# Kernel tuning notes

Hardware: AMD Instinct MI355X
Metric: run time of the kernel (lower is better)

Reference implementation:

```python
import jax, jax.numpy as jnp
import numpy as np

EMBED_DIM = 1024
NUM_HEADS = 16
NUM_GROUPS = 4
HEAD_DIM = EMBED_DIM // NUM_HEADS
REPEAT = NUM_HEADS // NUM_GROUPS
MAX_TIME = 128
MAX_FREQ = 8


def build_relative_index(q_len, k_len, freq_size=MAX_FREQ, max_time=MAX_TIME, max_freq=MAX_FREQ):
    # static (numpy) construction; shapes are compile-time constants under jit
    q_time = q_len // max_freq
    k_time = k_len // max_freq
    qt = np.arange(q_time) + (k_time - q_time)
    q_coords = np.stack(np.meshgrid(qt, np.arange(freq_size), indexing='ij')).reshape(2, -1)
    k_coords = np.stack(np.meshgrid(np.arange(k_time), np.arange(freq_size), indexing='ij')).reshape(2, -1)
    rel = q_coords[:, :, None] - k_coords[:, None, :]  # [2, Nq, Nk]
    rel_t = np.clip(rel[0], -max_time + 1, max_time - 1) + max_time - 1
    rel_f = np.clip(rel[1], -max_freq + 1, max_freq - 1) + max_freq - 1
    return jnp.asarray(rel_t, jnp.int32), jnp.asarray(rel_f, jnp.int32)


def setup_inputs() -> dict:
    key = jax.random.key(0)
    ks = jax.random.split(key, 11)
    B, N, D, Nc = 2, 512, EMBED_DIM, 1536
    s = 0.02
    return {
        'q': jax.random.normal(ks[0], (B, N, D), jnp.float32),
        'k': jax.random.normal(ks[1], (B, N, D), jnp.float32),
        'v': jax.random.normal(ks[2], (B, N, D), jnp.float32),
        'attn_cache_k': jax.random.normal(ks[3], (B * NUM_HEADS, HEAD_DIM, Nc), jnp.float32),
        'attn_cache_v': jax.random.normal(ks[4], (B * NUM_HEADS, Nc, HEAD_DIM), jnp.float32),
        'Wq': jax.random.normal(ks[5], (D, D), jnp.float32) * s,
        'Wk': jax.random.normal(ks[6], (D, HEAD_DIM * NUM_GROUPS), jnp.float32) * s,
        'Wv': jax.random.normal(ks[7], (D, HEAD_DIM * NUM_GROUPS), jnp.float32) * s,
        'Wo': jax.random.normal(ks[8], (D, D), jnp.float32) * s,
        'emb_t': jax.random.normal(ks[9], (2 * MAX_TIME - 1, HEAD_DIM), jnp.float32) * s,
        'emb_f': jax.random.normal(ks[10], (2 * MAX_FREQ - 1, HEAD_DIM), jnp.float32) * s,
    }


def reference(q, k, v, attn_cache_k, attn_cache_v, Wq, Wk, Wv, Wo, emb_t, emb_f):
    B, N, D = q.shape
    H, G, hd, r = NUM_HEADS, NUM_GROUPS, HEAD_DIM, REPEAT
    # projections (no bias); head layout matches torch view: [B, N, H, hd] -> [B*H, N, hd]
    qp = (q @ Wq).reshape(B, N, H, hd).transpose(0, 2, 1, 3).reshape(B * H, N, hd)
    kp = (k @ Wk).reshape(B, N, G, hd).transpose(0, 2, 3, 1).reshape(B * G, hd, N)  # transposed K
    vp = (v @ Wv).reshape(B, N, G, hd).transpose(0, 2, 1, 3).reshape(B * G, N, hd)
    # GQA: repeat_interleave kv heads to query heads
    kp = jnp.repeat(kp, r, axis=0)
    vp = jnp.repeat(vp, r, axis=0)
    # streaming cache concat + slide
    k_full = jnp.concatenate([attn_cache_k, kp], axis=-1)            # [B*H, hd, Nk]
    new_cache_k = k_full[:, :, -attn_cache_k.shape[-1]:]
    v_full = jnp.concatenate([attn_cache_v, vp], axis=1)             # [B*H, Nk, hd]
    new_cache_v = v_full[:, -attn_cache_v.shape[1]:, :]
    Nk = k_full.shape[-1]
    qs = qp * (hd ** -0.5)
    scores = jnp.einsum('bid,bdj->bij', qs, k_full)                  # [B*H, N, Nk]
    rel_t, rel_f = build_relative_index(N, Nk)
    rel_emb = emb_t[rel_t] + emb_f[rel_f]                            # [N, Nk, hd]
    bias = jnp.einsum('bid,ijd->bij', qs, rel_emb)
    attn = jax.nn.softmax(scores + bias, axis=-1)
    ao = jnp.einsum('bij,bjd->bid', attn, v_full)                    # [B*H, N, hd]
    ao = ao.reshape(B, H, N, hd).transpose(2, 0, 1, 3).reshape(N, B, D)
    out = (ao @ Wo).transpose(1, 0, 2)                               # [B, N, D]
    return out, new_cache_k, new_cache_v
```

## Files before the change

kernel.cpp:

```cpp
#include <hip/hip_runtime.h>
#include <math.h>

typedef _Float16 half_t;
typedef _Float16 half8  __attribute__((ext_vector_type(8)));
typedef _Float16 half4v __attribute__((ext_vector_type(4)));
typedef float    floatx4 __attribute__((ext_vector_type(4)));

#define LOG2E 1.44269504088896f

static __device__ __forceinline__ floatx4 mfma16(half8 a, half8 b, floatx4 c) {
    return __builtin_amdgcn_mfma_f32_16x16x32_f16(a, b, c, 0, 0, 0);
}
static __device__ __forceinline__ floatx4 mfma16x16(half4v a, half4v b, floatx4 c) {
    return __builtin_amdgcn_mfma_f32_16x16x16f16(a, b, c, 0, 0, 0);
}

__global__ __launch_bounds__(256) void prep(const float* __restrict__ cache_k,
                                            const float* __restrict__ cache_v,
                                            const float* __restrict__ Wq,
                                            const float* __restrict__ Wk,
                                            const float* __restrict__ Wv,
                                            const float* __restrict__ Wo,
                                            const float* __restrict__ emb_t,
                                            const float* __restrict__ emb_f,
                                            half_t* __restrict__ Kc,
                                            half_t* __restrict__ VcT,
                                            float* __restrict__ out_k,
                                            float* __restrict__ out_v,
                                            half_t* __restrict__ WqT,
                                            half_t* __restrict__ WkvT,
                                            half_t* __restrict__ WoT,
                                            half_t* __restrict__ embc)
{
    const int tid = threadIdx.x;
    const int z = blockIdx.z;
    __shared__ float t[64][65];
    if (z == 0) {
        const int bh = blockIdx.y, j0 = blockIdx.x * 64;
        const bool shift = (j0 >= 512);
        #pragma unroll
        for (int i2 = 0; i2 < 4; i2++) {
            int idx = i2 * 256 + tid;
            int d = idx >> 4, j4 = (idx & 15) * 4;
            float4 vv = *(const float4*)&cache_k[((size_t)bh * 64 + d) * 1536 + j0 + j4];
            *(float4*)&t[d][j4] = vv;
            if (shift) *(float4*)&out_k[((size_t)bh * 64 + d) * 1536 + j0 - 512 + j4] = vv;
        }
        __syncthreads();
        #pragma unroll
        for (int i2 = 0; i2 < 2; i2++) {
            int idx = i2 * 256 + tid;
            int j = idx >> 3, db = (idx & 7) * 8;
            half8 o;
            #pragma unroll
            for (int u = 0; u < 8; u++) o[u] = (half_t)t[db + u][j];
            *(half8*)&Kc[((size_t)bh * 1536 + j0 + j) * 64 + db] = o;
        }
    } else if (z == 1) {
        const int bh = blockIdx.y, j0 = blockIdx.x * 64;
        const bool shift = (j0 >= 512);
        #pragma unroll
        for (int i2 = 0; i2 < 4; i2++) {
            int idx = i2 * 256 + tid;
            int j = idx >> 4, d4 = (idx & 15) * 4;
            float4 vv = *(const float4*)&cache_v[((size_t)bh * 1536 + j0 + j) * 64 + d4];
            *(float4*)&t[j][d4] = vv;
            if (shift) *(float4*)&out_v[((size_t)bh * 1536 + j0 + j - 512) * 64 + d4] = vv;
        }
        __syncthreads();
        #pragma unroll
        for (int i2 = 0; i2 < 2; i2++) {
            int idx = i2 * 256 + tid;
            int d = idx >> 3, jb = (idx & 7) * 8;
            half8 o;
            #pragma unroll
            for (int u = 0; u < 8; u++) o[u] = (half_t)t[jb + u][d];
            *(half8*)&VcT[((size_t)bh * 64 + d) * 1536 + j0 + jb] = o;
        }
    } else {
        const int id = blockIdx.y * 24 + blockIdx.x;
        const float* src; half_t* dst; int Ncols, n0, k0;
        if (id < 256)      { src = Wq; dst = WqT; Ncols = 1024; n0 = (id & 15) * 64; k0 = (id >> 4) * 64; }
        else if (id < 320) { int q2 = id - 256; src = Wk; dst = WkvT; Ncols = 256; n0 = (q2 & 3) * 64; k0 = (q2 >> 2) * 64; }
        else if (id < 384) { int q2 = id - 320; src = Wv; dst = WkvT + 256 * 1024; Ncols = 256; n0 = (q2 & 3) * 64; k0 = (q2 >> 2) * 64; }
        else if (id < 640) { int q2 = id - 384; src = Wo; dst = WoT; Ncols = 1024; n0 = (q2 & 15) * 64; k0 = (q2 >> 4) * 64; }
        else if (id < 720) {
            int idx = (id - 640) * 256 + tid;
            int row = idx >> 6, col = idx & 63;
            float val = 0.f;
            if (row < 255) val = emb_t[row * 64 + col];
            else if (row >= 256 && row < 271) val = emb_f[(row - 256) * 64 + col];
            embc[idx] = (half_t)val;
            return;
        } else return;
        #pragma unroll
        for (int i2 = 0; i2 < 4; i2++) {
            int idx = i2 * 256 + tid;
            int r = idx >> 4, c4 = (idx & 15) * 4;
            *(float4*)&t[r][c4] = *(const float4*)&src[(size_t)(k0 + r) * Ncols + n0 + c4];
        }
        __syncthreads();
        #pragma unroll
        for (int i2 = 0; i2 < 2; i2++) {
            int idx = i2 * 256 + tid;
            int n = idx >> 3, kb = (idx & 7) * 8;
            half8 o;
            #pragma unroll
            for (int u = 0; u < 8; u++) o[u] = (half_t)t[kb + u][n];
            *(half8*)&dst[(size_t)(n0 + n) * 1024 + k0 + kb] = o;
        }
    }
}

__global__ __launch_bounds__(512) void proj(int phase,
                                            const float* __restrict__ qin,
                                            const float* __restrict__ kin,
                                            const float* __restrict__ vin,
                                            const half_t* __restrict__ AO,
                                            const half_t* __restrict__ WqT,
                                            const half_t* __restrict__ WkvT,
                                            const half_t* __restrict__ WoT,
                                            half_t* __restrict__ qs_h,
                                            half_t* __restrict__ kp_h,
                                            half_t* __restrict__ vpT,
                                            float* __restrict__ out,
                                            float* __restrict__ out_k,
                                            float* __restrict__ out_v)
{
    __shared__ __align__(16) half_t As[2][2][64 * 72];
    __shared__ __align__(16) half_t Bs[2][2][64 * 72];
    const int id = blockIdx.x;
    int task, m0, n0;
    const float* Af = nullptr; const half_t* Ah = nullptr; const half_t* Bt;
    if (phase == 1)      { task = 2; m0 = (id >> 4) * 64; n0 = (id & 15) * 64; Ah = AO; Bt = WoT; }
    else if (id < 256)   { task = 0; m0 = (id >> 4) * 64; n0 = (id & 15) * 64; Af = qin; Bt = WqT; }
    else { task = 1; int t = id - 256; m0 = (t >> 3) * 64; n0 = (t & 7) * 64;
           Af = (n0 < 256) ? kin : vin; Bt = WkvT; }

    const int tid = threadIdx.x;
    const int kh = tid >> 8, t8 = tid & 255;
    const int w4 = (tid >> 6) & 3, l = tid & 63;
    const int quad = l >> 4, lr = l & 15, wm = w4 >> 1, wn = w4 & 1;
    const int arow = t8 >> 2, acol = (t8 & 3) * 16;
    const int kbase = kh * 512;

    {
        int kk = kbase;
        if (Af) {
            float4 f0 = *(const float4*)&Af[(size_t)(m0 + arow) * 1024 + kk + acol];
            float4 f1 = *(const float4*)&Af[(size_t)(m0 + arow) * 1024 + kk + acol + 4];
            float4 f2 = *(const float4*)&Af[(size_t)(m0 + arow) * 1024 + kk + acol + 8];
            float4 f3 = *(const float4*)&Af[(size_t)(m0 + arow) * 1024 + kk + acol + 12];
            half8 h0, h1;
            h0[0]=(half_t)f0.x; h0[1]=(half_t)f0.y; h0[2]=(half_t)f0.z; h0[3]=(half_t)f0.w;
            h0[4]=(half_t)f1.x; h0[5]=(half_t)f1.y; h0[6]=(half_t)f1.z; h0[7]=(half_t)f1.w;
            h1[0]=(half_t)f2.x; h1[1]=(half_t)f2.y; h1[2]=(half_t)f2.z; h1[3]=(half_t)f2.w;
            h1[4]=(half_t)f3.x; h1[5]=(half_t)f3.y; h1[6]=(half_t)f3.z; h1[7]=(half_t)f3.w;
            *(half8*)&As[kh][0][arow * 72 + acol] = h0;
            *(half8*)&As[kh][0][arow * 72 + acol + 8] = h1;
        } else {
            *(half8*)&As[kh][0][arow * 72 + acol]     = *(const half8*)&Ah[(size_t)(m0 + arow) * 1024 + kk + acol];
            *(half8*)&As[kh][0][arow * 72 + acol + 8] = *(const half8*)&Ah[(size_t)(m0 + arow) * 1024 + kk + acol + 8];
        }
        *(half8*)&Bs[kh][0][arow * 72 + acol]     = *(const half8*)&Bt[(size_t)(n0 + arow) * 1024 + kk + acol];
        *(half8*)&Bs[kh][0][arow * 72 + acol + 8] = *(const half8*)&Bt[(size_t)(n0 + arow) * 1024 + kk + acol + 8];
    }
    __syncthreads();

    floatx4 zero = {0.f, 0.f, 0.f, 0.f};
    floatx4 acc[2][2];
    acc[0][0] = zero; acc[0][1] = zero; acc[1][0] = zero; acc[1][1] = zero;

    float4 pf0, pf1, pf2, pf3; half8 ph0, ph1, pb0, pb1;
    for (int it = 0; it < 8; ++it) {
        if (it < 7) {
            int kk = kbase + (it + 1) * 64;
            if (Af) {
                pf0 = *(const float4*)&Af[(size_t)(m0 + arow) * 1024 + kk + acol];
                pf1 = *(const float4*)&Af[(size_t)(m0 + arow) * 1024 + kk + acol + 4];
                pf2 = *(const float4*)&Af[(size_t)(m0 + arow) * 1024 + kk + acol + 8];
                pf3 = *(const float4*)&Af[(size_t)(m0 + arow) * 1024 + kk + acol + 12];
            } else {
                ph0 = *(const half8*)&Ah[(size_t)(m0 + arow) * 1024 + kk + acol];
                ph1 = *(const half8*)&Ah[(size_t)(m0 + arow) * 1024 + kk + acol + 8];
            }
            pb0 = *(const half8*)&Bt[(size_t)(n0 + arow) * 1024 + kk + acol];
            pb1 = *(const half8*)&Bt[(size_t)(n0 + arow) * 1024 + kk + acol + 8];
        }
        const half_t* Ab = &As[kh][it & 1][0];
        const half_t* Bb = &Bs[kh][it & 1][0];
        #pragma unroll
        for (int ks = 0; ks < 2; ++ks) {
            half8 a0 = *(const half8*)&Ab[(wm * 32 + lr) * 72 + ks * 32 + quad * 8];
            half8 a1 = *(const half8*)&Ab[(wm * 32 + 16 + lr) * 72 + ks * 32 + quad * 8];
            half8 b0 = *(const half8*)&Bb[(wn * 32 + lr) * 72 + ks * 32 + quad * 8];
            half8 b1 = *(const half8*)&Bb[(wn * 32 + 16 + lr) * 72 + ks * 32 + quad * 8];
            acc[0][0] = mfma16(a0, b0, acc[0][0]);
            acc[0][1] = mfma16(a0, b1, acc[0][1]);
            acc[1][0] = mfma16(a1, b0, acc[1][0]);
            acc[1][1] = mfma16(a1, b1, acc[1][1]);
        }
        __syncthreads();
        if (it < 7) {
            int buf = (it + 1) & 1;
            if (Af) {
                half8 h0, h1;
                h0[0]=(half_t)pf0.x; h0[1]=(half_t)pf0.y; h0[2]=(half_t)pf0.z; h0[3]=(half_t)pf0.w;
                h0[4]=(half_t)pf1.x; h0[5]=(half_t)pf1.y; h0[6]=(half_t)pf1.z; h0[7]=(half_t)pf1.w;
                h1[0]=(half_t)pf2.x; h1[1]=(half_t)pf2.y; h1[2]=(half_t)pf2.z; h1[3]=(half_t)pf2.w;
                h1[4]=(half_t)pf3.x; h1[5]=(half_t)pf3.y; h1[6]=(half_t)pf3.z; h1[7]=(half_t)pf3.w;
                *(half8*)&As[kh][buf][arow * 72 + acol] = h0;
                *(half8*)&As[kh][buf][arow * 72 + acol + 8] = h1;
            } else {
                *(half8*)&As[kh][buf][arow * 72 + acol] = ph0;
                *(half8*)&As[kh][buf][arow * 72 + acol + 8] = ph1;
            }
            *(half8*)&Bs[kh][buf][arow * 72 + acol] = pb0;
            *(half8*)&Bs[kh][buf][arow * 72 + acol + 8] = pb1;
            __syncthreads();
        }
    }

    float* M = (float*)&Bs[0][0][0];
    if (kh == 1) {
        #pragma unroll
        for (int mi = 0; mi < 2; mi++)
            #pragma unroll
            for (int ni = 0; ni < 2; ni++)
                #pragma unroll
                for (int r = 0; r < 4; r++)
                    M[(wm * 32 + mi * 16 + quad * 4 + r) * 66 + wn * 32 + ni * 16 + lr] = acc[mi][ni][r];
    }
    __syncthreads();
    if (kh == 0) {
        #pragma unroll
        for (int mi = 0; mi < 2; mi++)
            #pragma unroll
            for (int ni = 0; ni < 2; ni++)
                #pragma unroll
                for (int r = 0; r < 4; r++)
                    acc[mi][ni][r] += M[(wm * 32 + mi * 16 + quad * 4 + r) * 66 + wn * 32 + ni * 16 + lr];
    }

    if (task == 0) {
        if (kh == 0) {
            #pragma unroll
            for (int mi = 0; mi < 2; mi++)
                #pragma unroll
                for (int ni = 0; ni < 2; ni++)
                    #pragma unroll
                    for (int r = 0; r < 4; r++) {
                        int m = m0 + wm * 32 + mi * 16 + quad * 4 + r;
                        int n = n0 + wn * 32 + ni * 16 + lr;
                        qs_h[(size_t)m * 1024 + n] = (half_t)(acc[mi][ni][r] * (0.125f * LOG2E));
                    }
        }
    } else if (task == 2) {
        if (kh == 0) {
            #pragma unroll
            for (int mi = 0; mi < 2; mi++)
                #pragma unroll
                for (int ni = 0; ni < 2; ni++)
                    #pragma unroll
                    for (int r = 0; r < 4; r++) {
                        int m = m0 + wm * 32 + mi * 16 + quad * 4 + r;
                        int n = n0 + wn * 32 + ni * 16 + lr;
                        out[(size_t)m * 1024 + n] = acc[mi][ni][r];
                    }
        }
    } else {
        float* Ct = (float*)&As[0][0][0];
        if (kh == 0) {
            #pragma unroll
            for (int mi = 0; mi < 2; mi++)
                #pragma unroll
                for (int ni = 0; ni < 2; ni++)
                    #pragma unroll
                    for (int r = 0; r < 4; r++)
                        Ct[(wn * 32 + ni * 16 + lr) * 68 + wm * 32 + mi * 16 + quad * 4 + r] = acc[mi][ni][r];
        }
        __syncthreads();
        if (kh == 0) {
            const int b = m0 >> 9, jm0 = m0 & 511;
            if (n0 < 256) {
                int gg = n0 >> 6;
                {
                    int d = t8 >> 2, jc = (t8 & 3) * 16;
                    float4 vv[4];
                    #pragma unroll
                    for (int u = 0; u < 4; u++) vv[u] = *(float4*)&Ct[d * 68 + jc + u * 4];
                    #pragma unroll
                    for (int t = 0; t < 4; t++)
                        #pragma unroll
                        for (int u = 0; u < 4; u++)
                            *(float4*)&out_k[((size_t)((b * 16 + gg * 4 + t) * 64 + d)) * 1536 + 1024 + jm0 + jc + u * 4] = vv[u];
                }
                {
                    int j = t8 >> 2, dc = (t8 & 3) * 16;
                    half8 o0, o1;
                    #pragma unroll
                    for (int u = 0; u < 8; u++) o0[u] = (half_t)Ct[(dc + u) * 68 + j];
                    #pragma unroll
                    for (int u = 0; u < 8; u++) o1[u] = (half_t)Ct[(dc + 8 + u) * 68 + j];
                    *(half8*)&kp_h[((size_t)(b * 512 + jm0 + j)) * 256 + n0 + dc] = o0;
                    *(half8*)&kp_h[((size_t)(b * 512 + jm0 + j)) * 256 + n0 + dc + 8] = o1;
                }
            } else {
                int gg = (n0 - 256) >> 6;
                {
                    int j = t8 >> 2, dc = (t8 & 3) * 16;
                    float4 vv[4];
                    #pragma unroll
                    for (int u = 0; u < 4; u++) {
                        float4 x;
                        x.x = Ct[(dc + u * 4 + 0) * 68 + j];
                        x.y = Ct[(dc + u * 4 + 1) * 68 + j];
                        x.z = Ct[(dc + u * 4 + 2) * 68 + j];
                        x.w = Ct[(dc + u * 4 + 3) * 68 + j];
                        vv[u] = x;
                    }
                    #pragma unroll
                    for (int t = 0; t < 4; t++)
                        #pragma unroll
                        for (int u = 0; u < 4; u++)
                            *(float4*)&out_v[(((size_t)(b * 16 + gg * 4 + t) * 1536) + 1024 + jm0 + j) * 64 + dc + u * 4] = vv[u];
                }
                {
                    int d = t8 >> 2, jc = (t8 & 3) * 16;
                    half8 o0, o1;
                    #pragma unroll
                    for (int u = 0; u < 8; u++) o0[u] = (half_t)Ct[d * 68 + jc + u];
                    #pragma unroll
                    for (int u = 0; u < 8; u++) o1[u] = (half_t)Ct[d * 68 + jc + 8 + u];
                    *(half8*)&vpT[((size_t)((b * 4 + gg) * 64 + d)) * 512 + jm0 + jc] = o0;
                    *(half8*)&vpT[((size_t)((b * 4 + gg) * 64 + d)) * 512 + jm0 + jc + 8] = o1;
                }
            }
        }
    }
}

__global__ __launch_bounds__(512, 4) void flash(const half_t* __restrict__ qs_h,
                                                const half_t* __restrict__ Kc,
                                                const half_t* __restrict__ kp_h,
                                                const half_t* __restrict__ VcT,
                                                const half_t* __restrict__ vpT,
                                                const half_t* __restrict__ embc,
                                                half_t* __restrict__ AO)
{
    __shared__ __align__(16) half_t smem[25152];
    half_t* Ks = smem;
    half_t* Vs = smem + 8192;
    half_t* Qs = smem + 16384;
    half_t* bt = smem + 18432;

    const int bh = blockIdx.x, b = bh >> 4, h = bh & 15, g = h >> 2;
    const int i0 = blockIdx.y * 32;
    const int tid = threadIdx.x, w = tid >> 6, l = tid & 63;
    const int quad = l >> 4, lr = l & 15;
    const int wq = w >> 2, jh = w & 3;

    if (tid < 256) {
        int row = tid >> 3, cc = tid & 7;
        *(half8*)&Qs[row * 64 + ((cc ^ (row & 7)) * 8)] =
            *(const half8*)&qs_h[((size_t)(b * 512 + i0 + row)) * 1024 + h * 64 + cc * 8];
    }

    half8 kr[2], vr[2];
    #pragma unroll
    for (int u = 0; u < 2; u++) {
        int row = u * 64 + (tid >> 3);
        kr[u] = *(const half8*)&Kc[((size_t)bh * 1536 + row) * 64 + (tid & 7) * 8];
        int d = u * 32 + (tid >> 4);
        vr[u] = *(const half8*)&VcT[((size_t)bh * 64 + d) * 1536 + (tid & 15) * 8];
    }
    __syncthreads();

    half8 qf0 = *(const half8*)&Qs[(wq * 16 + lr) * 64 + ((quad ^ (lr & 7)) * 8)];
    half8 qf1 = *(const half8*)&Qs[(wq * 16 + lr) * 64 + (((4 + quad) ^ (lr & 7)) * 8)];

    floatx4 zero = {0.f, 0.f, 0.f, 0.f};
    for (int tk = 4 + jh; tk < 17; tk += 4) {
        floatx4 acc = zero;
        half8 e0 = *(const half8*)&embc[(size_t)(tk * 16 + lr) * 64 + quad * 8];
        half8 e1 = *(const half8*)&embc[(size_t)(tk * 16 + lr) * 64 + 32 + quad * 8];
        acc = mfma16(e0, qf0, acc);
        acc = mfma16(e1, qf1, acc);
        #pragma unroll
        for (int r = 0; r < 4; r++)
            bt[(wq * 16 + lr) * 210 + tk * 16 + quad * 4 + r - 64] = (half_t)acc[r];
    }

    #pragma unroll
    for (int u = 0; u < 2; u++) {
        int row = u * 64 + (tid >> 3);
        *(half8*)&Ks[row * 64 + (((tid & 7) ^ (row & 7)) * 8)] = kr[u];
        int d = u * 32 + (tid >> 4);
        *(half8*)&Vs[d * 128 + (((tid & 15) ^ (d & 7)) * 8)] = vr[u];
    }
    __syncthreads();

    const int qtr = (i0 + wq * 16 + lr) >> 3;
    float bfv[4];
    #pragma unroll
    for (int r = 0; r < 4; r++) {
        int f = (lr & 7) - ((quad & 1) * 4 + r) + 7;
        bfv[r] = (float)bt[(wq * 16 + lr) * 210 + 192 + f];
    }

    floatx4 accO[4];
    #pragma unroll
    for (int ni = 0; ni < 4; ni++) accO[ni] = zero;
    floatx4 accS = zero;
    const half4v vone = {(half_t)1.f, (half_t)1.f, (half_t)1.f, (half_t)1.f};

    for (int jt = 0; jt < 16; ++jt) {
        if (jt < 15) {
            const int j1 = (jt + 1) * 128;
            #pragma unroll
            for (int u = 0; u < 2; u++) {
                int row = u * 64 + (tid >> 3);
                const half_t* ksrc = (j1 < 1536)
                    ? &Kc[((size_t)bh * 1536 + j1 + row) * 64 + (tid & 7) * 8]
                    : &kp_h[((size_t)(b * 512 + j1 - 1536 + row)) * 256 + g * 64 + (tid & 7) * 8];
                kr[u] = *(const half8*)ksrc;
                int d = u * 32 + (tid >> 4);
                const half_t* vsrc = (j1 < 1536)
                    ? &VcT[((size_t)bh * 64 + d) * 1536 + j1 + (tid & 15) * 8]
                    : &vpT[((size_t)(b * 4 + g) * 64 + d) * 512 + (j1 - 1536) + (tid & 15) * 8];
                vr[u] = *(const half8*)vsrc;
            }
        }

        floatx4 s[2];
        #pragma unroll
        for (int c = 0; c < 2; c++) {
            int row = jh * 32 + c * 16 + lr;
            half8 kf0 = *(const half8*)&Ks[row * 64 + ((quad ^ (row & 7)) * 8)];
            half8 kf1 = *(const half8*)&Ks[row * 64 + (((4 + quad) ^ (row & 7)) * 8)];
            s[c] = mfma16(kf0, qf0, zero);
            s[c] = mfma16(kf1, qf1, s[c]);
        }
        const int ktb = jt * 16 + jh * 4 + (quad >> 1);
        const half_t* btrow = &bt[(wq * 16 + lr) * 210];
        #pragma unroll
        for (int c = 0; c < 2; c++) {
            int toff = 255 + qtr - (ktb + c * 2);
            toff = min(toff, 190);
            float tb = (float)btrow[toff];
            #pragma unroll
            for (int r = 0; r < 4; r++)
                s[c][r] = exp2f(s[c][r] + tb + bfv[r]);
        }
        #pragma unroll
        for (int c = 0; c < 2; c++) {
            half4v pf;
            #pragma unroll
            for (int r = 0; r < 4; r++) pf[r] = (half_t)s[c][r];
            accS = mfma16x16(pf, vone, accS);
            const int bj = jh * 4 + c * 2 + (quad >> 1);
            #pragma unroll
            for (int ni = 0; ni < 4; ni++) {
                int d = ni * 16 + lr;
                half4v vb = *(const half4v*)&Vs[d * 128 + ((bj ^ (lr & 7)) * 8) + (quad & 1) * 4];
                accO[ni] = mfma16x16(pf, vb, accO[ni]);
            }
        }
        __syncthreads();
        if (jt < 15) {
            #pragma unroll
            for (int u = 0; u < 2; u++) {
                int row = u * 64 + (tid >> 3);
                *(half8*)&Ks[row * 64 + (((tid & 7) ^ (row & 7)) * 8)] = kr[u];
                int d = u * 32 + (tid >> 4);
                *(half8*)&Vs[d * 128 + (((tid & 15) ^ (d & 7)) * 8)] = vr[u];
            }
            __syncthreads();
        }
    }

    float* Mf = (float*)smem;
    float* Sf = Mf + 6 * 16 * 68;
    if (jh != 0) {
        int p = (jh - 1) * 2 + wq;
        #pragma unroll
        for (int ni = 0; ni < 4; ni++)
            #pragma unroll
            for (int r = 0; r < 4; r++)
                Mf[(p * 16 + quad * 4 + r) * 68 + ni * 16 + lr] = accO[ni][r];
        if (lr == 0) {
            #pragma unroll
            for (int r = 0; r < 4; r++)
                Sf[p * 16 + quad * 4 + r] = accS[r];
        }
    }
    __syncthreads();
    if (jh == 0) {
        float inv[4];
        #pragma unroll
        for (int r = 0; r < 4; r++) {
            float t = accS[r];
            #pragma unroll
            for (int jj = 0; jj < 3; jj++) t += Sf[(jj * 2 + wq) * 16 + quad * 4 + r];
            inv[r] = 1.0f / t;
        }
        #pragma unroll
        for (int ni = 0; ni < 4; ni++)
            #pragma unroll
            for (int r = 0; r < 4; r++) {
                float o = accO[ni][r];
                #pragma unroll
                for (int jj = 0; jj < 3; jj++)
                    o += Mf[((jj * 2 + wq) * 16 + quad * 4 + r) * 68 + ni * 16 + lr];
                int row = wq * 16 + quad * 4 + r;
                AO[((size_t)(b * 512 + i0 + row)) * 1024 + h * 64 + ni * 16 + lr] =
                    (half_t)(o * inv[r]);
            }
    }
}

extern "C" void kernel_launch(void* const* d_in, const int* in_sizes, int n_in,
                              void* d_out, int out_size, void* d_ws, size_t ws_size,
                              hipStream_t stream)
{
    const float* q       = (const float*)d_in[0];
    const float* k       = (const float*)d_in[1];
    const float* v       = (const float*)d_in[2];
    const float* cache_k = (const float*)d_in[3];
    const float* cache_v = (const float*)d_in[4];
    const float* Wq      = (const float*)d_in[5];
    const float* Wk      = (const float*)d_in[6];
    const float* Wv      = (const float*)d_in[7];
    const float* Wo      = (const float*)d_in[8];
    const float* emb_t   = (const float*)d_in[9];
    const float* emb_f   = (const float*)d_in[10];

    float* out   = (float*)d_out;
    float* out_k = out + 1048576;
    float* out_v = out_k + 3145728;

    half_t* ws = (half_t*)d_ws;
    half_t* qs_h = ws;
    half_t* kp_h = ws + 1048576;
    half_t* vpT  = ws + 1310720;
    half_t* Kc   = ws + 1572864;
    half_t* VcT  = ws + 4718592;
    half_t* WqT  = ws + 7864320;
    half_t* WkvT = ws + 8912896;
    half_t* WoT  = ws + 9437184;
    half_t* embc = ws + 10485760;
    half_t* AO   = ws + 10506240;

    prep<<<dim3(24, 32, 3), 256, 0, stream>>>(cache_k, cache_v, Wq, Wk, Wv, Wo,
                                              emb_t, emb_f, Kc, VcT, out_k, out_v,
                                              WqT, WkvT, WoT, embc);
    proj<<<dim3(384), 512, 0, stream>>>(0, q, k, v, nullptr, WqT, WkvT, WoT,
                                        qs_h, kp_h, vpT, out, out_k, out_v);
    flash<<<dim3(32, 16), 512, 0, stream>>>(qs_h, Kc, kp_h, VcT, vpT, embc, AO);
    proj<<<dim3(256), 512, 0, stream>>>(1, q, k, v, AO, WqT, WkvT, WoT,
                                        qs_h, kp_h, vpT, out, out_k, out_v);
}
```

Baseline: 168.4 us.

## Load K/V fragments straight from global in MFMA-ready layout, drop LDS staging

The V cache and projected V are now stored in a 4-key-interleaved layout ([j/4][d][4]), so each lane can load its MFMA B operand with a single half4 global read. The flash kernel no longer stages K/V tiles in shared memory and drops the per-tile barriers. Each of the 8 warps now handles all 32 query rows over a 16-key slice, with a 7-way reduction at the end. This removes LDS traffic and synchronisation from the inner loop. In exchange it issues many small uncoalesced-ish global loads that rely on L2/cache, and it uses more registers and a larger final reduction.

Measured after the change: 174.7 us. 1.04x slower.

```diff
diff --git a/kernel.cpp b/kernel.cpp
--- a/kernel.cpp
+++ b/kernel.cpp
@@ -24,7 +24,7 @@
                                             const float* __restrict__ emb_t,
                                             const float* __restrict__ emb_f,
                                             half_t* __restrict__ Kc,
-                                            half_t* __restrict__ VcT,
+                                            half_t* __restrict__ Vc4,
                                             float* __restrict__ out_k,
                                             float* __restrict__ out_v,
                                             half_t* __restrict__ WqT,
@@ -69,13 +69,13 @@
         }
         __syncthreads();
         #pragma unroll
-        for (int i2 = 0; i2 < 2; i2++) {
+        for (int i2 = 0; i2 < 4; i2++) {
             int idx = i2 * 256 + tid;
-            int d = idx >> 3, jb = (idx & 7) * 8;
-            half8 o;
-            #pragma unroll
-            for (int u = 0; u < 8; u++) o[u] = (half_t)t[jb + u][d];
-            *(half8*)&VcT[((size_t)bh * 64 + d) * 1536 + j0 + jb] = o;
+            int jc = idx >> 6, d = idx & 63;
+            half4v o;
+            #pragma unroll
+            for (int u = 0; u < 4; u++) o[u] = (half_t)t[jc * 4 + u][d];
+            *(half4v*)&Vc4[(((size_t)bh * 384 + (j0 >> 2) + jc) * 64 + d) * 4] = o;
         }
     } else {
         const int id = blockIdx.y * 24 + blockIdx.x;
@@ -122,7 +122,7 @@
                                             const half_t* __restrict__ WoT,
                                             half_t* __restrict__ qs_h,
                                             half_t* __restrict__ kp_h,
-                                            half_t* __restrict__ vpT,
+                                            half_t* __restrict__ Vp4,
                                             float* __restrict__ out,
                                             float* __restrict__ out_k,
                                             float* __restrict__ out_v)
@@ -326,14 +326,14 @@
                             *(float4*)&out_v[(((size_t)(b * 16 + gg * 4 + t) * 1536) + 1024 + jm0 + j) * 64 + dc + u * 4] = vv[u];
                 }
                 {
-                    int d = t8 >> 2, jc = (t8 & 3) * 16;
-                    half8 o0, o1;
-                    #pragma unroll
-                    for (int u = 0; u < 8; u++) o0[u] = (half_t)Ct[d * 68 + jc + u];
-                    #pragma unroll
-                    for (int u = 0; u < 8; u++) o1[u] = (half_t)Ct[d * 68 + jc + 8 + u];
-                    *(half8*)&vpT[((size_t)((b * 4 + gg) * 64 + d)) * 512 + jm0 + jc] = o0;
-                    *(half8*)&vpT[((size_t)((b * 4 + gg) * 64 + d)) * 512 + jm0 + jc + 8] = o1;
+                    int d = t8 >> 2, jc16 = (t8 & 3) * 16;
+                    #pragma unroll
+                    for (int u = 0; u < 4; u++) {
+                        half4v o;
+                        #pragma unroll
+                        for (int s2 = 0; s2 < 4; s2++) o[s2] = (half_t)Ct[d * 68 + jc16 + u * 4 + s2];
+                        *(half4v*)&Vp4[(((size_t)(b * 4 + gg) * 128 + ((jm0 + jc16) >> 2) + u) * 64 + d) * 4] = o;
+                    }
                 }
             }
         }
@@ -343,179 +343,165 @@
 __global__ __launch_bounds__(512, 4) void flash(const half_t* __restrict__ qs_h,
                                                 const half_t* __restrict__ Kc,
                                                 const half_t* __restrict__ kp_h,
-                                                const half_t* __restrict__ VcT,
-                                                const half_t* __restrict__ vpT,
+                                                const half_t* __restrict__ Vc4,
+                                                const half_t* __restrict__ Vp4,
                                                 const half_t* __restrict__ embc,
                                                 half_t* __restrict__ AO)
 {
-    __shared__ __align__(16) half_t smem[25152];
-    half_t* Ks = smem;
-    half_t* Vs = smem + 8192;
-    half_t* Qs = smem + 16384;
-    half_t* bt = smem + 18432;
+    __shared__ __align__(16) unsigned char smem_raw[61824];
+    half_t* bt = (half_t*)smem_raw;
 
     const int bh = blockIdx.x, b = bh >> 4, h = bh & 15, g = h >> 2;
     const int i0 = blockIdx.y * 32;
-    const int tid = threadIdx.x, w = tid >> 6, l = tid & 63;
+    const int tid = threadIdx.x, jh = tid >> 6, l = tid & 63;
     const int quad = l >> 4, lr = l & 15;
-    const int wq = w >> 2, jh = w & 3;
-
-    if (tid < 256) {
-        int row = tid >> 3, cc = tid & 7;
-        *(half8*)&Qs[row * 64 + ((cc ^ (row & 7)) * 8)] =
-            *(const half8*)&qs_h[((size_t)(b * 512 + i0 + row)) * 1024 + h * 64 + cc * 8];
-    }
-
-    half8 kr[2], vr[2];
+
+    half8 qf[2][2];
     #pragma unroll
-    for (int u = 0; u < 2; u++) {
-        int row = u * 64 + (tid >> 3);
-        kr[u] = *(const half8*)&Kc[((size_t)bh * 1536 + row) * 64 + (tid & 7) * 8];
-        int d = u * 32 + (tid >> 4);
-        vr[u] = *(const half8*)&VcT[((size_t)bh * 64 + d) * 1536 + (tid & 15) * 8];
+    for (int ih = 0; ih < 2; ih++) {
+        const half_t* qsrc = &qs_h[((size_t)(b * 512 + i0 + ih * 16 + lr)) * 1024 + h * 64];
+        qf[ih][0] = *(const half8*)(qsrc + quad * 8);
+        qf[ih][1] = *(const half8*)(qsrc + 32 + quad * 8);
+    }
+
+    floatx4 zero = {0.f, 0.f, 0.f, 0.f};
+    {
+        int ih = jh & 1;
+        for (int tk = 4 + (jh >> 1); tk < 17; tk += 4) {
+            floatx4 acc = zero;
+            half8 e0 = *(const half8*)&embc[(size_t)(tk * 16 + lr) * 64 + quad * 8];
+            half8 e1 = *(const half8*)&embc[(size_t)(tk * 16 + lr) * 64 + 32 + quad * 8];
+            acc = mfma16(e0, qf[ih][0], acc);
+            acc = mfma16(e1, qf[ih][1], acc);
+            #pragma unroll
+            for (int r = 0; r < 4; r++)
+                bt[(ih * 16 + lr) * 210 + tk * 16 + quad * 4 + r - 64] = (half_t)acc[r];
+        }
     }
     __syncthreads();
 
-    half8 qf0 = *(const half8*)&Qs[(wq * 16 + lr) * 64 + ((quad ^ (lr & 7)) * 8)];
-    half8 qf1 = *(const half8*)&Qs[(wq * 16 + lr) * 64 + (((4 + quad) ^ (lr & 7)) * 8)];
-
-    floatx4 zero = {0.f, 0.f, 0.f, 0.f};
-    for (int tk = 4 + jh; tk < 17; tk += 4) {
-        floatx4 acc = zero;
-        half8 e0 = *(const half8*)&embc[(size_t)(tk * 16 + lr) * 64 + quad * 8];
-        half8 e1 = *(const half8*)&embc[(size_t)(tk * 16 + lr) * 64 + 32 + quad * 8];
-        acc = mfma16(e0, qf0, acc);
-        acc = mfma16(e1, qf1, acc);
-        #pragma unroll
-        for (int r = 0; r < 4; r++)
-            bt[(wq * 16 + lr) * 210 + tk * 16 + quad * 4 + r - 64] = (half_t)acc[r];
-    }
-
+    float bfv[2][4];
     #pragma unroll
-    for (int u = 0; u < 2; u++) {
-        int row = u * 64 + (tid >> 3);
-        *(half8*)&Ks[row * 64 + (((tid & 7) ^ (row & 7)) * 8)] = kr[u];
-        int d = u * 32 + (tid >> 4);
-        *(half8*)&Vs[d * 128 + (((tid & 15) ^ (d & 7)) * 8)] = vr[u];
-    }
+    for (int ih = 0; ih < 2; ih++)
+        #pragma unroll
+        for (int r = 0; r < 4; r++) {
+            int f = (lr & 7) - ((quad & 1) * 4 + r) + 7;
+            bfv[ih][r] = (float)bt[(ih * 16 + lr) * 210 + 192 + f];
+        }
+    const int qtr0 = (i0 + lr) >> 3;
+    const int qtr1 = (i0 + 16 + lr) >> 3;
+
+    floatx4 accO[2][4];
+    #pragma unroll
+    for (int ih = 0; ih < 2; ih++)
+        #pragma unroll
+        for (int ni = 0; ni < 4; ni++) accO[ih][ni] = zero;
+    floatx4 accS[2];
+    accS[0] = zero; accS[1] = zero;
+    const half4v vone = {(half_t)1.f, (half_t)1.f, (half_t)1.f, (half_t)1.f};
+
+    half8 kc0, kc1;
+    {
+        const half_t* kb = &Kc[((size_t)bh * 1536 + jh * 16 + lr) * 64];
+        kc0 = *(const half8*)(kb + quad * 8);
+        kc1 = *(const half8*)(kb + 32 + quad * 8);
+    }
+
+    for (int jt = 0; jt < 16; ++jt) {
+        const int j0 = jt * 128;
+        half4v vb[4];
+        {
+            const half_t* vbase; int jcb;
+            if (j0 < 1536) { vbase = Vc4 + (size_t)bh * 98304;          jcb = j0 >> 2; }
+            else           { vbase = Vp4 + (size_t)(b * 4 + g) * 32768; jcb = (j0 - 1536) >> 2; }
+            const int jc = jcb + jh * 4 + quad;
+            #pragma unroll
+            for (int ni = 0; ni < 4; ni++)
+                vb[ni] = *(const half4v*)&vbase[((size_t)jc * 64 + ni * 16 + lr) * 4];
+        }
+        half8 kn0, kn1;
+        if (jt < 15) {
+            const int j1 = j0 + 128;
+            const half_t* kb = (j1 < 1536)
+                ? &Kc[((size_t)bh * 1536 + j1 + jh * 16 + lr) * 64]
+                : &kp_h[((size_t)(b * 512 + j1 - 1536 + jh * 16 + lr)) * 256 + g * 64];
+            kn0 = *(const half8*)(kb + quad * 8);
+            kn1 = *(const half8*)(kb + 32 + quad * 8);
+        }
+
+        floatx4 s[2];
+        #pragma unroll
+        for (int ih = 0; ih < 2; ih++) {
+            s[ih] = mfma16(kc0, qf[ih][0], zero);
+            s[ih] = mfma16(kc1, qf[ih][1], s[ih]);
+        }
+        const int ktb = jt * 16 + jh * 2 + (quad >> 1);
+        #pragma unroll
+        for (int ih = 0; ih < 2; ih++) {
+            int toff = 255 + (ih ? qtr1 : qtr0) - ktb;
+            toff = min(toff, 190);
+            float tb = (float)bt[(ih * 16 + lr) * 210 + toff];
+            #pragma unroll
+            for (int r = 0; r < 4; r++)
+                s[ih][r] = exp2f(s[ih][r] + tb + bfv[ih][r]);
+        }
+        #pragma unroll
+        for (int ih = 0; ih < 2; ih++) {
+            half4v pf;
+            #pragma unroll
+            for (int r = 0; r < 4; r++) pf[r] = (half_t)s[ih][r];
+            accS[ih] = mfma16x16(pf, vone, accS[ih]);
+            #pragma unroll
+            for (int ni = 0; ni < 4; ni++)
+                accO[ih][ni] = mfma16x16(pf, vb[ni], accO[ih][ni]);
+        }
+        if (jt < 15) { kc0 = kn0; kc1 = kn1; }
+    }
+
     __syncthreads();
-
-    const int qtr = (i0 + wq * 16 + lr) >> 3;
-    float bfv[4];
-    #pragma unroll
-    for (int r = 0; r < 4; r++) {
-        int f = (lr & 7) - ((quad & 1) * 4 + r) + 7;
-        bfv[r] = (float)bt[(wq * 16 + lr) * 210 + 192 + f];
-    }
-
-    floatx4 accO[4];
-    #pragma unroll
-    for (int ni = 0; ni < 4; ni++) accO[ni] = zero;
-    floatx4 accS = zero;
-    const half4v vone = {(half_t)1.f, (half_t)1.f, (half_t)1.f, (half_t)1.f};
-
-    for (int jt = 0; jt < 16; ++jt) {
-        if (jt < 15) {
-            const int j1 = (jt + 1) * 128;
-            #pragma unroll
-            for (int u = 0; u < 2; u++) {
-                int row = u * 64 + (tid >> 3);
-                const half_t* ksrc = (j1 < 1536)
-                    ? &Kc[((size_t)bh * 1536 + j1 + row) * 64 + (tid & 7) * 8]
-                    : &kp_h[((size_t)(b * 512 + j1 - 1536 + row)) * 256 + g * 64 + (tid & 7) * 8];
-                kr[u] = *(const half8*)ksrc;
-                int d = u * 32 + (tid >> 4);
-                const half_t* vsrc = (j1 < 1536)
-                    ? &VcT[((size_t)bh * 64 + d) * 1536 + j1 + (tid & 15) * 8]
-                    : &vpT[((size_t)(b * 4 + g) * 64 + d) * 512 + (j1 - 1536) + (tid & 15) * 8];
-                vr[u] = *(const half8*)vsrc;
+    float* Mf = (float*)smem_raw;
+    float* Sf = Mf + 7 * 32 * 68;
+    if (jh != 0) {
+        const int p = jh - 1;
+        #pragma unroll
+        for (int ih = 0; ih < 2; ih++) {
+            #pragma unroll
+            for (int ni = 0; ni < 4; ni++)
+                #pragma unroll
+                for (int r = 0; r < 4; r++)
+                    Mf[(p * 32 + ih * 16 + quad * 4 + r) * 68 + ni * 16 + lr] = accO[ih][ni][r];
+            if (lr == 0) {
+                #pragma unroll
+                for (int r = 0; r < 4; r++)
+                    Sf[p * 32 + ih * 16 + quad * 4 + r] = accS[ih][r];
             }
-        }
-
-        floatx4 s[2];
-        #pragma unroll
-        for (int c = 0; c < 2; c++) {
-            int row = jh * 32 + c * 16 + lr;
-            half8 kf0 = *(const half8*)&Ks[row * 64 + ((quad ^ (row & 7)) * 8)];
-            half8 kf1 = *(const half8*)&Ks[row * 64 + (((4 + quad) ^ (row & 7)) * 8)];
-            s[c] = mfma16(kf0, qf0, zero);
-            s[c] = mfma16(kf1, qf1, s[c]);
-        }
-        const int ktb = jt * 16 + jh * 4 + (quad >> 1);
-        const half_t* btrow = &bt[(wq * 16 + lr) * 210];
-        #pragma unroll
-        for (int c = 0; c < 2; c++) {
-            int toff = 255 + qtr - (ktb + c * 2);
-            toff = min(toff, 190);
-            float tb = (float)btrow[toff];
-            #pragma unroll
-            for (int r = 0; r < 4; r++)
-                s[c][r] = exp2f(s[c][r] + tb + bfv[r]);
-        }
-        #pragma unroll
-        for (int c = 0; c < 2; c++) {
-            half4v pf;
-            #pragma unroll
-            for (int r = 0; r < 4; r++) pf[r] = (half_t)s[c][r];
-            accS = mfma16x16(pf, vone, accS);
-            const int bj = jh * 4 + c * 2 + (quad >> 1);
-            #pragma unroll
-            for (int ni = 0; ni < 4; ni++) {
-                int d = ni * 16 + lr;
-                half4v vb = *(const half4v*)&Vs[d * 128 + ((bj ^ (lr & 7)) * 8) + (quad & 1) * 4];
-                accO[ni] = mfma16x16(pf, vb, accO[ni]);
-            }
-        }
-        __syncthreads();
-        if (jt < 15) {
-            #pragma unroll
-            for (int u = 0; u < 2; u++) {
-                int row = u * 64 + (tid >> 3);
-                *(half8*)&Ks[row * 64 + (((tid & 7) ^ (row & 7)) * 8)] = kr[u];
-                int d = u * 32 + (tid >> 4);
-                *(half8*)&Vs[d * 128 + (((tid & 15) ^ (d & 7)) * 8)] = vr[u];
-            }
-            __syncthreads();
-        }
-    }
-
-    float* Mf = (float*)smem;
-    float* Sf = Mf + 6 * 16 * 68;
-    if (jh != 0) {
-        int p = (jh - 1) * 2 + wq;
-        #pragma unroll
-        for (int ni = 0; ni < 4; ni++)
-            #pragma unroll
-            for (int r = 0; r < 4; r++)
-                Mf[(p * 16 + quad * 4 + r) * 68 + ni * 16 + lr] = accO[ni][r];
-        if (lr == 0) {
-            #pragma unroll
-            for (int r = 0; r < 4; r++)
-                Sf[p * 16 + quad * 4 + r] = accS[r];
         }
     }
     __syncthreads();
     if (jh == 0) {
-        float inv[4];
-        #pragma unroll
-        for (int r = 0; r < 4; r++) {
-            float t = accS[r];
-            #pragma unroll
-            for (int jj = 0; jj < 3; jj++) t += Sf[(jj * 2 + wq) * 16 + quad * 4 + r];
-            inv[r] = 1.0f / t;
-        }
-        #pragma unroll
-        for (int ni = 0; ni < 4; ni++)
+        #pragma unroll
+        for (int ih = 0; ih < 2; ih++) {
+            float inv[4];
             #pragma unroll
             for (int r = 0; r < 4; r++) {
-                float o = accO[ni][r];
-                #pragma unroll
-                for (int jj = 0; jj < 3; jj++)
-                    o += Mf[((jj * 2 + wq) * 16 + quad * 4 + r) * 68 + ni * 16 + lr];
-                int row = wq * 16 + quad * 4 + r;
-                AO[((size_t)(b * 512 + i0 + row)) * 1024 + h * 64 + ni * 16 + lr] =
-                    (half_t)(o * inv[r]);
+                float t = accS[ih][r];
+                #pragma unroll
+                for (int p = 0; p < 7; p++) t += Sf[p * 32 + ih * 16 + quad * 4 + r];
+                inv[r] = 1.0f / t;
             }
+            #pragma unroll
+            for (int ni = 0; ni < 4; ni++)
+                #pragma unroll
+                for (int r = 0; r < 4; r++) {
+                    float o = accO[ih][ni][r];
+                    #pragma unroll
+                    for (int p = 0; p < 7; p++)
+                        o += Mf[(p * 32 + ih * 16 + quad * 4 + r) * 68 + ni * 16 + lr];
+                    int row = ih * 16 + quad * 4 + r;
+                    AO[((size_t)(b * 512 + i0 + row)) * 1024 + h * 64 + ni * 16 + lr] =
+                        (half_t)(o * inv[r]);
+                }
+        }
     }
 }
 
@@ -542,9 +528,9 @@
     half_t* ws = (half_t*)d_ws;
     half_t* qs_h = ws;
     half_t* kp_h = ws + 1048576;
-    half_t* vpT  = ws + 1310720;
+    half_t* Vp4  = ws + 1310720;
     half_t* Kc   = ws + 1572864;
-    half_t* VcT  = ws + 4718592;
+    half_t* Vc4  = ws + 4718592;
     half_t* WqT  = ws + 7864320;
     half_t* WkvT = ws + 8912896;
     half_t* WoT  = ws + 9437184;
@@ -552,11 +538,11 @@
     half_t* AO   = ws + 10506240;
 
     prep<<<dim3(24, 32, 3), 256, 0, stream>>>(cache_k, cache_v, Wq, Wk, Wv, Wo,
-                                              emb_t, emb_f, Kc, VcT, out_k, out_v,
+                                              emb_t, emb_f, Kc, Vc4, out_k, out_v,
                                               WqT, WkvT, WoT, embc);
     proj<<<dim3(384), 512, 0, stream>>>(0, q, k, v, nullptr, WqT, WkvT, WoT,
-                                        qs_h, kp_h, vpT, out, out_k, out_v);
-    flash<<<dim3(32, 16), 512, 0, stream>>>(qs_h, Kc, kp_h, VcT, vpT, embc, AO);
+                                        qs_h, kp_h, Vp4, out, out_k, out_v);
+    flash<<<dim3(32, 16), 512, 0, stream>>>(qs_h, Kc, kp_h, Vc4, Vp4, embc, AO);
     proj<<<dim3(256), 512, 0, stream>>>(1, q, k, v, AO, WqT, WkvT, WoT,
-                                        qs_h, kp_h, vpT, out, out_k, out_v);
+                                        qs_h, kp_h, Vp4, out, out_k, out_v);
 }
```
